# Performance work log

Hardware: AMD Instinct MI355X
Metric: run time of the kernel (lower is better)

The kernel has to match this reference:

```python
import jax, jax.numpy as jnp
from jax import lax
import numpy as np

N, T, D, H, HG, OG = 2048, 256, 16, 256, 256, 128

def setup_inputs() -> dict:
    key = jax.random.key(0)
    ks = jax.random.split(key, 16)
    s = 0.05
    return {
        'x':    jax.random.normal(ks[0], (N, T, D), jnp.float32),
        'Wih0': jax.random.normal(ks[1], (4 * H, D), jnp.float32) * s,
        'Whh0': jax.random.normal(ks[2], (4 * H, H), jnp.float32) * s,
        'bih0': jax.random.normal(ks[3], (4 * H,), jnp.float32) * s,
        'bhh0': jax.random.normal(ks[4], (4 * H,), jnp.float32) * s,
        'Wih1': jax.random.normal(ks[5], (4 * H, H), jnp.float32) * s,
        'Whh1': jax.random.normal(ks[6], (4 * H, H), jnp.float32) * s,
        'bih1': jax.random.normal(ks[7], (4 * H,), jnp.float32) * s,
        'bhh1': jax.random.normal(ks[8], (4 * H,), jnp.float32) * s,
        'Wg1':  jax.random.normal(ks[9], (H, HG), jnp.float32) * s,
        'Wg2':  jax.random.normal(ks[10], (HG, OG), jnp.float32) * s,
        'Wfc':  jax.random.normal(ks[11], (OG, 1), jnp.float32) * s,
        'bfc':  jax.random.normal(ks[12], (1,), jnp.float32) * s,
    }

def lstm_layer(x, Wih, Whh, bih, bhh):
    # x: [N, T, Din]; torch gate order i, f, g, o stacked along 4H
    n = x.shape[0]
    h4 = Whh.shape[0]
    hid = h4 // 4
    xg = jnp.einsum('ntd,gd->ntg', x, Wih) + bih + bhh  # precompute input part
    def step(carry, g_t):
        h, c = carry
        g = g_t + h @ Whh.T
        i, f, gg, o = jnp.split(g, 4, axis=-1)
        c = jax.nn.sigmoid(f) * c + jax.nn.sigmoid(i) * jnp.tanh(gg)
        h = jax.nn.sigmoid(o) * jnp.tanh(c)
        return (h, c), h
    h0 = jnp.zeros((n, hid), x.dtype)
    (_, _), hs = lax.scan(step, (h0, h0), jnp.swapaxes(xg, 0, 1))
    return jnp.swapaxes(hs, 0, 1)  # [N, T, H]

def adjacency(nf):
    # detached correlation graph + symmetric degree normalization
    f = lax.stop_gradient(nf)
    xc = f - f.mean(axis=1, keepdims=True)
    cov = xc @ xc.T
    d = jnp.sqrt(jnp.diag(cov))
    corr = jnp.nan_to_num(jnp.clip(cov / (d[:, None] * d[None, :]), -1.0, 1.0))
    A = corr + jnp.eye(f.shape[0], dtype=f.dtype)
    dinv = jnp.power(A.sum(axis=1), -0.5)
    dinv = jnp.where(jnp.isinf(dinv), 0.0, dinv)
    return dinv[:, None] * A * dinv[None, :]

def reference(x, Wih0, Whh0, bih0, bhh0, Wih1, Whh1, bih1, bhh1, Wg1, Wg2, Wfc, bfc):
    h = lstm_layer(x, Wih0, Whh0, bih0, bhh0)
    h = lstm_layer(h, Wih1, Whh1, bih1, bhh1)
    nf = h[:, -1, :]                      # [N, H]
    adj = adjacency(nf)                   # [N, N]
    g1 = jax.nn.relu(adj @ (nf @ Wg1))    # GCN layer 1 (dropout=0, eval)
    g2 = adj @ (g1 @ Wg2)                 # GCN layer 2
    pred = g2 @ Wfc + bfc                 # [N, 1]
    return pred[:, 0]
```

## Files before the change

kernel.cpp:

```cpp
#include <hip/hip_runtime.h>
#include <hip/hip_bf16.h>
#include <cmath>

#define NN 2048
#define TT 256
#define DD 16
#define HH 256
#define NBLK 512

typedef __attribute__((ext_vector_type(8))) short short8;
typedef __attribute__((ext_vector_type(4))) float f32x4;

__device__ __forceinline__ float sigmoidf_(float x){ return 1.0f/(1.0f+expf(-x)); }

__device__ __forceinline__ void glds16(const __hip_bfloat16* g, __hip_bfloat16* l){
  __builtin_amdgcn_global_load_lds(
      (const __attribute__((address_space(1))) void*)g,
      (__attribute__((address_space(3))) void*)l, 16, 0, 0);
}
__device__ __forceinline__ void glds16_dev(const __hip_bfloat16* g, __hip_bfloat16* l){
  __builtin_amdgcn_global_load_lds(
      (const __attribute__((address_space(1))) void*)g,
      (__attribute__((address_space(3))) void*)l, 16, 0, 17);
}

__global__ __launch_bounds__(256) void pack_w2(const float* __restrict__ W,
                                               __hip_bfloat16* __restrict__ P){
  int tid = blockIdx.x*256 + threadIdx.x;
  int r = tid >> 8, k = tid & 255;
  float w = W[tid];
  __hip_bfloat16 h = __float2bfloat16(w);
  __hip_bfloat16 l = __float2bfloat16(w - __bfloat162float(h));
  size_t base = (size_t)r*512;
  P[base + k] = h; P[base + 256 + k] = l;
}
__global__ __launch_bounds__(256) void pack_w0(const float* __restrict__ W,
                                               __hip_bfloat16* __restrict__ P){
  int tid = blockIdx.x*256 + threadIdx.x;
  int r = tid >> 4, k = tid & 15;
  float w = W[tid];
  __hip_bfloat16 h = __float2bfloat16(w);
  __hip_bfloat16 l = __float2bfloat16(w - __bfloat162float(h));
  size_t base = (size_t)r*64;
  P[base + k] = h; P[base + 16 + k] = h; P[base + 32 + k] = l;
  P[base + 48 + k] = __float2bfloat16(0.0f);
}
__global__ __launch_bounds__(256) void pack_x(const float* __restrict__ x,
                                              __hip_bfloat16* __restrict__ Xp){
  int tid = blockIdx.x*256 + threadIdx.x;
  const float* xr = x + (size_t)tid*16;
  __hip_bfloat16* o = Xp + (size_t)tid*64;
  for (int k=0;k<16;k++){
    float v = xr[k];
    __hip_bfloat16 h = __float2bfloat16(v);
    __hip_bfloat16 l = __float2bfloat16(v - __bfloat162float(h));
    o[k] = h; o[16+k] = l; o[32+k] = h; o[48+k] = __float2bfloat16(0.0f);
  }
}
__global__ __launch_bounds__(256) void recon_nf(const __hip_bfloat16* __restrict__ hi,
    const __hip_bfloat16* __restrict__ lo, float* __restrict__ nf){
  int tid = blockIdx.x*256 + threadIdx.x;
  nf[tid] = __bfloat162float(hi[tid]) + __bfloat162float(lo[tid]);
}

__global__ __launch_bounds__(256) void bar_init(unsigned* __restrict__ bar){
  for (int i = threadIdx.x; i < 2048; i += 256) bar[i] = 0u;
}

__device__ __forceinline__ void lean_sync(unsigned* bar, int t, int bid){
  __syncthreads();
  if (threadIdx.x == 0){
    const int x = bid & 7;
    unsigned a = __hip_atomic_fetch_add(bar + x*16, 1u, __ATOMIC_RELAXED,
                                        __HIP_MEMORY_SCOPE_AGENT);
    if (a == (unsigned)(64u*(t+1) - 1u)){
      unsigned g = __hip_atomic_fetch_add(bar + 128, 1u, __ATOMIC_RELAXED,
                                          __HIP_MEMORY_SCOPE_AGENT);
      if (g == (unsigned)(8u*(t+1) - 1u)){
        #pragma unroll
        for (int i=0;i<8;i++)
          __hip_atomic_store(bar + 1536 + i*64, (unsigned)(t+1),
                             __ATOMIC_RELAXED, __HIP_MEMORY_SCOPE_AGENT);
      } else {
        while (__hip_atomic_load(bar + 1536 + x*64, __ATOMIC_RELAXED,
                                 __HIP_MEMORY_SCOPE_AGENT) < (unsigned)(t+1))
          __builtin_amdgcn_s_sleep(4);
      }
    } else {
      while (__hip_atomic_load(bar + 1536 + x*64, __ATOMIC_RELAXED,
                               __HIP_MEMORY_SCOPE_AGENT) < (unsigned)(t+1))
        __builtin_amdgcn_s_sleep(4);
    }
  }
  __syncthreads();
}

__device__ __forceinline__ void mm_merged(
    const __hip_bfloat16* __restrict__ Ahi, const __hip_bfloat16* __restrict__ Alo,
    size_t lda,
    const __hip_bfloat16* __restrict__ Bhi, const __hip_bfloat16* __restrict__ Blo,
    size_t ldb, int Klen,
    int m0, int j0, int wv, int lane, int rr, int sw8, int frow,
    f32x4 (&acc)[2][4],
    __hip_bfloat16* AsH, __hip_bfloat16* AsL,
    __hip_bfloat16* BsH, __hip_bfloat16* BsL)
{
  const size_t arow = (size_t)(m0 + wv*32 + rr)*lda + sw8;
  const size_t brow = (size_t)(wv*256 + j0 + rr)*ldb + sw8;
  for (int kb=0; kb<Klen; kb+=64){
    {
      const __hip_bfloat16* AbH = Ahi + arow + kb;
      __hip_bfloat16* AdH = AsH + (wv*32)*64;
      #pragma unroll
      for (int c2=0;c2<4;c2++) glds16_dev(AbH + (size_t)(c2*8)*lda, AdH + c2*8*64);
      const __hip_bfloat16* AbL = Alo + arow + kb;
      __hip_bfloat16* AdL = AsL + (wv*32)*64;
      #pragma unroll
      for (int c2=0;c2<4;c2++) glds16_dev(AbL + (size_t)(c2*8)*lda, AdL + c2*8*64);
      const __hip_bfloat16* Bb1 = Bhi + brow + kb;
      __hip_bfloat16* Bd1 = BsH + (wv<<4)*64;
      glds16(Bb1, Bd1); glds16(Bb1 + (size_t)8*ldb, Bd1 + 8*64);
      const __hip_bfloat16* Bb2 = Blo + brow + kb;
      __hip_bfloat16* Bd2 = BsL + (wv<<4)*64;
      glds16(Bb2, Bd2); glds16(Bb2 + (size_t)8*ldb, Bd2 + 8*64);
    }
    __syncthreads();
    #pragma unroll
    for (int w2=0; w2<2; ++w2){
      const int sl8 = ((((w2<<2) + (lane>>4)) ^ (lane&7)) << 3);
      short8 ah0 = *(const short8*)&AsH[(wv*32 +      frow)*64 + sl8];
      short8 ah1 = *(const short8*)&AsH[(wv*32 + 16 + frow)*64 + sl8];
      short8 al0 = *(const short8*)&AsL[(wv*32 +      frow)*64 + sl8];
      short8 al1 = *(const short8*)&AsL[(wv*32 + 16 + frow)*64 + sl8];
      #pragma unroll
      for (int g=0; g<4; ++g){
        short8 bh = *(const short8*)&BsH[((g<<4) + frow)*64 + sl8];
        acc[0][g] = __builtin_amdgcn_mfma_f32_16x16x32_bf16(ah0, bh, acc[0][g], 0,0,0);
        acc[1][g] = __builtin_amdgcn_mfma_f32_16x16x32_bf16(ah1, bh, acc[1][g], 0,0,0);
        acc[0][g] = __builtin_amdgcn_mfma_f32_16x16x32_bf16(al0, bh, acc[0][g], 0,0,0);
        acc[1][g] = __builtin_amdgcn_mfma_f32_16x16x32_bf16(al1, bh, acc[1][g], 0,0,0);
        short8 bl = *(const short8*)&BsL[((g<<4) + frow)*64 + sl8];
        acc[0][g] = __builtin_amdgcn_mfma_f32_16x16x32_bf16(ah0, bl, acc[0][g], 0,0,0);
        acc[1][g] = __builtin_amdgcn_mfma_f32_16x16x32_bf16(ah1, bl, acc[1][g], 0,0,0);
      }
    }
    __syncthreads();
  }
}

__device__ __forceinline__ void mm_single64(
    const __hip_bfloat16* __restrict__ A, size_t lda,
    const __hip_bfloat16* __restrict__ B, size_t ldb,
    int m0, int j0, int wv, int lane, int rr, int sw8, int frow,
    f32x4 (&acc)[2][4],
    __hip_bfloat16* As0, __hip_bfloat16* Bh0)
{
  {
    const __hip_bfloat16* Ab = A + (size_t)(m0 + wv*32 + rr)*lda + sw8;
    __hip_bfloat16* Ad = As0 + (wv*32)*64;
    #pragma unroll
    for (int c2=0;c2<4;c2++) glds16(Ab + (size_t)(c2*8)*lda, Ad + c2*8*64);
    const __hip_bfloat16* Bb1 = B + (size_t)(wv*256 + j0 + rr)*ldb + sw8;
    __hip_bfloat16* Bd1 = Bh0 + (wv<<4)*64;
    glds16(Bb1, Bd1); glds16(Bb1 + (size_t)8*ldb, Bd1 + 8*64);
  }
  __syncthreads();
  #pragma unroll
  for (int w2=0; w2<2; ++w2){
    const int sl8 = ((((w2<<2) + (lane>>4)) ^ (lane&7)) << 3);
    short8 a0 = *(const short8*)&As0[(wv*32 +      frow)*64 + sl8];
    short8 a1 = *(const short8*)&As0[(wv*32 + 16 + frow)*64 + sl8];
    #pragma unroll
    for (int g=0; g<4; ++g){
      short8 b1 = *(const short8*)&Bh0[((g<<4) + frow)*64 + sl8];
      acc[0][g] = __builtin_amdgcn_mfma_f32_16x16x32_bf16(a0, b1, acc[0][g], 0,0,0);
      acc[1][g] = __builtin_amdgcn_mfma_f32_16x16x32_bf16(a1, b1, acc[1][g], 0,0,0);
    }
  }
  __syncthreads();
}

__global__ __launch_bounds__(256, 2) void lstm2_all(
    const __hip_bfloat16* __restrict__ Xp,
    const __hip_bfloat16* __restrict__ P0ih,
    const __hip_bfloat16* __restrict__ P0hh,
    const __hip_bfloat16* __restrict__ P1ih,
    const __hip_bfloat16* __restrict__ P1hh,
    const float* __restrict__ bih0, const float* __restrict__ bhh0,
    const float* __restrict__ bih1, const float* __restrict__ bhh1,
    __hip_bfloat16* __restrict__ H0hi0, __hip_bfloat16* __restrict__ H0lo0,
    __hip_bfloat16* __restrict__ H0hi1, __hip_bfloat16* __restrict__ H0lo1,
    __hip_bfloat16* __restrict__ H1hi0, __hip_bfloat16* __restrict__ H1lo0,
    __hip_bfloat16* __restrict__ H1hi1, __hip_bfloat16* __restrict__ H1lo1,
    unsigned* __restrict__ bar)
{
  __shared__ __align__(16) __hip_bfloat16 AsH[128*64];
  __shared__ __align__(16) __hip_bfloat16 AsL[128*64];
  __shared__ __align__(16) __hip_bfloat16 BsH[64*64];
  __shared__ __align__(16) __hip_bfloat16 BsL[64*64];

  const int bid = blockIdx.x;
  const int xcd = bid & 7;
  const int slot = bid >> 3;
  const bool isL0 = xcd < 4;
  const int lg = isL0 ? xcd : (xcd - 4);
  const int jg = ((lg & 1) << 3) + (slot & 7);
  const int mg = ((lg >> 1) << 3) + (slot >> 3);
  const int m0 = mg << 7;
  const int j0 = jg << 4;
  const int lane = threadIdx.x & 63, wv = threadIdx.x >> 6;
  const int rr = lane >> 3;
  const int sw8 = (((lane & 7) ^ rr) << 3);
  const int frow = lane & 15;
  const int odd = frow & 1;

  const int j = j0 + frow;
  const float* bih = isL0 ? bih0 : bih1;
  const float* bhh = isL0 ? bhh0 : bhh1;
  const float b0 = bih[j]        + bhh[j];
  const float b1 = bih[HH + j]   + bhh[HH + j];
  const float b2 = bih[2*HH + j] + bhh[2*HH + j];
  const float b3 = bih[3*HH + j] + bhh[3*HH + j];

  float creg[2][4] = {{0.f,0.f,0.f,0.f},{0.f,0.f,0.f,0.f}};

  for (int t = 0; t <= TT; ++t){
    const int p = t & 1;
    const bool active = isL0 ? (t < TT) : (t >= 1);
    if (active){
      f32x4 acc[2][4] = {};
      const __hip_bfloat16* h0p_hi = p ? H0hi0 : H0hi1;
      const __hip_bfloat16* h0p_lo = p ? H0lo0 : H0lo1;
      if (isL0){
        if (t != 0){
          mm_merged(h0p_hi, h0p_lo, 256, P0hh, P0hh+256, 512, 256,
                    m0, j0, wv, lane, rr, sw8, frow, acc, AsH, AsL, BsH, BsL);
        }
        mm_single64(Xp + (size_t)t*64, (size_t)TT*64, P0ih, 64,
                    m0, j0, wv, lane, rr, sw8, frow, acc, AsH, BsH);
      } else {
        mm_merged(h0p_hi, h0p_lo, 256, P1ih, P1ih+256, 512, 256,
                  m0, j0, wv, lane, rr, sw8, frow, acc, AsH, AsL, BsH, BsL);
        if (t != 1){
          const __hip_bfloat16* h1p_hi = p ? H1hi1 : H1hi0;
          const __hip_bfloat16* h1p_lo = p ? H1lo1 : H1lo0;
          mm_merged(h1p_hi, h1p_lo, 256, P1hh, P1hh+256, 512, 256,
                    m0, j0, wv, lane, rr, sw8, frow, acc, AsH, AsL, BsH, BsL);
        }
      }
      __hip_bfloat16* ohi = isL0 ? (p ? H0hi1 : H0hi0)
                                 : (p ? H1hi0 : H1hi1);
      __hip_bfloat16* olo = isL0 ? (p ? H0lo1 : H0lo0)
                                 : (p ? H1lo0 : H1lo1);
      #pragma unroll
      for (int mt=0; mt<2; ++mt){
        const int mrb = m0 + wv*32 + mt*16 + ((lane>>4)<<2);
        #pragma unroll
        for (int r=0; r<4; ++r){
          float gi = acc[mt][0][r] + b0;
          float gf = acc[mt][1][r] + b1;
          float gg = acc[mt][2][r] + b2;
          float go = acc[mt][3][r] + b3;
          float cn = sigmoidf_(gf)*creg[mt][r] + sigmoidf_(gi)*tanhf(gg);
          creg[mt][r] = cn;
          float hv = sigmoidf_(go)*tanhf(cn);
          __hip_bfloat16 hb = __float2bfloat16(hv);
          __hip_bfloat16 lb = __float2bfloat16(hv - __bfloat162float(hb));
          unsigned hs = (unsigned)*reinterpret_cast<unsigned short*>(&hb);
          unsigned ls = (unsigned)*reinterpret_cast<unsigned short*>(&lb);
          unsigned hp = (unsigned)__shfl_xor((int)hs, 1);
          unsigned lp = (unsigned)__shfl_xor((int)ls, 1);
          const size_t base = (size_t)(mrb + r)*HH + (size_t)(j & ~1);
          if (!odd){
            unsigned v = hs | (hp << 16);
            __hip_atomic_store((unsigned*)(ohi + base), v,
                               __ATOMIC_RELAXED, __HIP_MEMORY_SCOPE_AGENT);
          } else {
            unsigned v = lp | (ls << 16);
            __hip_atomic_store((unsigned*)(olo + base), v,
                               __ATOMIC_RELAXED, __HIP_MEMORY_SCOPE_AGENT);
          }
        }
      }
    }
    if (t < TT) lean_sync(bar, t, bid);
  }
}

__global__ __launch_bounds__(256) void gemm_nn(
    float* __restrict__ C, const float* __restrict__ A, const float* __restrict__ B,
    int K, int lda, int ldb, int ldc, int relu)
{
  __shared__ float As_[16][68];
  __shared__ float Bs_[16][64];
  float acc[4][4] = {};
  const int tx = threadIdx.x;
  const int m0 = blockIdx.y<<6, n0 = blockIdx.x<<6;
  const int am = tx>>2, ak = (tx&3)<<2;
  const int bk = tx>>4, bn = (tx&15)<<2;
  const int mm = (tx>>4)<<2, nc = (tx&15)<<2;
  for (int kb=0; kb<K; kb+=16){
    float4 av = *reinterpret_cast<const float4*>(A + (size_t)(m0+am)*lda + kb + ak);
    As_[ak][am]=av.x; As_[ak+1][am]=av.y; As_[ak+2][am]=av.z; As_[ak+3][am]=av.w;
    *reinterpret_cast<float4*>(&Bs_[bk][bn]) =
      *reinterpret_cast<const float4*>(B + (size_t)(kb+bk)*ldb + n0 + bn);
    __syncthreads();
    #pragma unroll
    for (int k=0;k<16;k++){
      float4 a4 = *reinterpret_cast<const float4*>(&As_[k][mm]);
      float4 b4 = *reinterpret_cast<const float4*>(&Bs_[k][nc]);
      acc[0][0]=fmaf(a4.x,b4.x,acc[0][0]); acc[0][1]=fmaf(a4.x,b4.y,acc[0][1]);
      acc[0][2]=fmaf(a4.x,b4.z,acc[0][2]); acc[0][3]=fmaf(a4.x,b4.w,acc[0][3]);
      acc[1][0]=fmaf(a4.y,b4.x,acc[1][0]); acc[1][1]=fmaf(a4.y,b4.y,acc[1][1]);
      acc[1][2]=fmaf(a4.y,b4.z,acc[1][2]); acc[1][3]=fmaf(a4.y,b4.w,acc[1][3]);
      acc[2][0]=fmaf(a4.z,b4.x,acc[2][0]); acc[2][1]=fmaf(a4.z,b4.y,acc[2][1]);
      acc[2][2]=fmaf(a4.z,b4.z,acc[2][2]); acc[2][3]=fmaf(a4.z,b4.w,acc[2][3]);
      acc[3][0]=fmaf(a4.w,b4.x,acc[3][0]); acc[3][1]=fmaf(a4.w,b4.y,acc[3][1]);
      acc[3][2]=fmaf(a4.w,b4.z,acc[3][2]); acc[3][3]=fmaf(a4.w,b4.w,acc[3][3]);
    }
    __syncthreads();
  }
  #pragma unroll
  for (int r=0;r<4;r++){
    float4 v = make_float4(acc[r][0],acc[r][1],acc[r][2],acc[r][3]);
    if (relu){ v.x=fmaxf(v.x,0.f); v.y=fmaxf(v.y,0.f); v.z=fmaxf(v.z,0.f); v.w=fmaxf(v.w,0.f); }
    *reinterpret_cast<float4*>(C + (size_t)(m0+mm+r)*ldc + n0 + nc) = v;
  }
}

__global__ __launch_bounds__(256) void gemm_nt(
    float* __restrict__ C, const float* __restrict__ A, const float* __restrict__ B,
    int K, int lda, int ldb, int ldc)
{
  __shared__ float As_[16][68];
  __shared__ float Bs_[16][68];
  float acc[4][4] = {};
  const int tx = threadIdx.x;
  const int m0 = blockIdx.y<<6, n0 = blockIdx.x<<6;
  const int am = tx>>2, ak = (tx&3)<<2;
  const int mm = (tx>>4)<<2, nc = (tx&15)<<2;
  for (int kb=0; kb<K; kb+=16){
    float4 av = *reinterpret_cast<const float4*>(A + (size_t)(m0+am)*lda + kb + ak);
    As_[ak][am]=av.x; As_[ak+1][am]=av.y; As_[ak+2][am]=av.z; As_[ak+3][am]=av.w;
    float4 bv = *reinterpret_cast<const float4*>(B + (size_t)(n0+am)*ldb + kb + ak);
    Bs_[ak][am]=bv.x; Bs_[ak+1][am]=bv.y; Bs_[ak+2][am]=bv.z; Bs_[ak+3][am]=bv.w;
    __syncthreads();
    #pragma unroll
    for (int k=0;k<16;k++){
      float4 a4 = *reinterpret_cast<const float4*>(&As_[k][mm]);
      float4 b4 = *reinterpret_cast<const float4*>(&Bs_[k][nc]);
      acc[0][0]=fmaf(a4.x,b4.x,acc[0][0]); acc[0][1]=fmaf(a4.x,b4.y,acc[0][1]);
      acc[0][2]=fmaf(a4.x,b4.z,acc[0][2]); acc[0][3]=fmaf(a4.x,b4.w,acc[0][3]);
      acc[1][0]=fmaf(a4.y,b4.x,acc[1][0]); acc[1][1]=fmaf(a4.y,b4.y,acc[1][1]);
      acc[1][2]=fmaf(a4.y,b4.z,acc[1][2]); acc[1][3]=fmaf(a4.y,b4.w,acc[1][3]);
      acc[2][0]=fmaf(a4.z,b4.x,acc[2][0]); acc[2][1]=fmaf(a4.z,b4.y,acc[2][1]);
      acc[2][2]=fmaf(a4.z,b4.z,acc[2][2]); acc[2][3]=fmaf(a4.z,b4.w,acc[2][3]);
      acc[3][0]=fmaf(a4.w,b4.x,acc[3][0]); acc[3][1]=fmaf(a4.w,b4.y,acc[3][1]);
      acc[3][2]=fmaf(a4.w,b4.z,acc[3][2]); acc[3][3]=fmaf(a4.w,b4.w,acc[3][3]);
    }
    __syncthreads();
  }
  #pragma unroll
  for (int r=0;r<4;r++){
    float4 v = make_float4(acc[r][0],acc[r][1],acc[r][2],acc[r][3]);
    *reinterpret_cast<float4*>(C + (size_t)(m0+mm+r)*ldc + n0 + nc) = v;
  }
}

__global__ __launch_bounds__(256) void rowstat(const float* __restrict__ nf,
    float* __restrict__ xc, float* __restrict__ dvec)
{
  __shared__ float red[256];
  int n = blockIdx.x, tx = threadIdx.x;
  float v = nf[(size_t)n*HH + tx];
  red[tx] = v; __syncthreads();
  for (int s=128; s>0; s>>=1){ if (tx<s) red[tx]+=red[tx+s]; __syncthreads(); }
  float mean = red[0] * (1.0f/HH);
  __syncthreads();
  float d = v - mean;
  xc[(size_t)n*HH + tx] = d;
  red[tx] = d*d; __syncthreads();
  for (int s=128; s>0; s>>=1){ if (tx<s) red[tx]+=red[tx+s]; __syncthreads(); }
  if (tx==0) dvec[n] = sqrtf(red[0]);
}

__global__ __launch_bounds__(256) void rowsum(const float* __restrict__ cov,
    const float* __restrict__ dvec, float* __restrict__ dinv)
{
  __shared__ float red[256];
  int i = blockIdx.x, tx = threadIdx.x;
  float di = dvec[i];
  float s = 0.f;
  for (int jj=tx; jj<NN; jj+=256){
    float r = cov[(size_t)i*NN + jj] / (di * dvec[jj]);
    if (r != r) r = 0.f; else r = fminf(1.f, fmaxf(-1.f, r));
    s += r;
  }
  red[tx]=s; __syncthreads();
  for (int st=128; st>0; st>>=1){ if (tx<st) red[tx]+=red[tx+st]; __syncthreads(); }
  if (tx==0){
    float tot = red[0] + 1.0f;
    float p = powf(tot, -0.5f);
    if (isinf(p)) p = 0.f;
    dinv[i] = p;
  }
}

__global__ __launch_bounds__(256) void adjnorm(float* __restrict__ cov,
    const float* __restrict__ dvec, const float* __restrict__ dinv)
{
  size_t idx = (size_t)blockIdx.x*256 + threadIdx.x;
  int i = (int)(idx >> 11), jj = (int)(idx & (NN-1));
  float r = cov[idx] / (dvec[i]*dvec[jj]);
  if (r != r) r = 0.f; else r = fminf(1.f, fmaxf(-1.f, r));
  if (i==jj) r += 1.f;
  cov[idx] = dinv[i]*r*dinv[jj];
}

__global__ __launch_bounds__(128) void predk(const float* __restrict__ G2,
    const float* __restrict__ Wfc, const float* __restrict__ bfc, float* __restrict__ out)
{
  int n = blockIdx.x, tx = threadIdx.x;
  float v = G2[(size_t)n*128 + tx] * Wfc[tx];
  for (int off=32; off>0; off>>=1) v += __shfl_down(v, off);
  __shared__ float p[2];
  if ((tx&63)==0) p[tx>>6] = v;
  __syncthreads();
  if (tx==0) out[n] = p[0] + p[1] + bfc[0];
}

extern "C" void kernel_launch(void* const* d_in, const int* in_sizes, int n_in,
                              void* d_out, int out_size, void* d_ws, size_t ws_size,
                              hipStream_t stream)
{
  const float* x    = (const float*)d_in[0];
  const float* Wih0 = (const float*)d_in[1];
  const float* Whh0 = (const float*)d_in[2];
  const float* bih0 = (const float*)d_in[3];
  const float* bhh0 = (const float*)d_in[4];
  const float* Wih1 = (const float*)d_in[5];
  const float* Whh1 = (const float*)d_in[6];
  const float* bih1 = (const float*)d_in[7];
  const float* bhh1 = (const float*)d_in[8];
  const float* Wg1  = (const float*)d_in[9];
  const float* Wg2  = (const float*)d_in[10];
  const float* Wfc  = (const float*)d_in[11];
  const float* bfc  = (const float*)d_in[12];
  float* out = (float*)d_out;

  char* w = (char*)d_ws;
  auto alloc = [&](size_t bytes){ char* p = w; w += (bytes + 255) & ~(size_t)255; return p; };
  __hip_bfloat16* Xp   = (__hip_bfloat16*)alloc((size_t)NN*TT*64*2);
  __hip_bfloat16* P0hh = (__hip_bfloat16*)alloc((size_t)1024*512*2);
  __hip_bfloat16* P1ih = (__hip_bfloat16*)alloc((size_t)1024*512*2);
  __hip_bfloat16* P1hh = (__hip_bfloat16*)alloc((size_t)1024*512*2);
  __hip_bfloat16* P0ih = (__hip_bfloat16*)alloc((size_t)1024*64*2);
  __hip_bfloat16 *H0hi[2], *H0lo[2], *H1hi[2], *H1lo[2];
  for (int i=0;i<2;i++){ H0hi[i]=(__hip_bfloat16*)alloc((size_t)NN*HH*2);
                         H0lo[i]=(__hip_bfloat16*)alloc((size_t)NN*HH*2); }
  for (int i=0;i<2;i++){ H1hi[i]=(__hip_bfloat16*)alloc((size_t)NN*HH*2);
                         H1lo[i]=(__hip_bfloat16*)alloc((size_t)NN*HH*2); }
  float* nf   = (float*)alloc((size_t)NN*HH*4);
  float* xc   = (float*)alloc((size_t)NN*HH*4);
  float* cov  = (float*)alloc((size_t)NN*NN*4);
  float* t1   = (float*)alloc((size_t)NN*HH*4);
  float* G1   = (float*)alloc((size_t)NN*HH*4);
  float* t2   = (float*)alloc((size_t)NN*128*4);
  float* G2   = (float*)alloc((size_t)NN*128*4);
  float* dvec = (float*)alloc((size_t)NN*4);
  float* dinv = (float*)alloc((size_t)NN*4);
  unsigned* bar = (unsigned*)alloc(8192);

  hipLaunchKernelGGL(bar_init, dim3(1), dim3(256), 0, stream, bar);
  hipLaunchKernelGGL(pack_w2, dim3(1024), dim3(256), 0, stream, Whh0, P0hh);
  hipLaunchKernelGGL(pack_w2, dim3(1024), dim3(256), 0, stream, Wih1, P1ih);
  hipLaunchKernelGGL(pack_w2, dim3(1024), dim3(256), 0, stream, Whh1, P1hh);
  hipLaunchKernelGGL(pack_w0, dim3(64),   dim3(256), 0, stream, Wih0, P0ih);
  hipLaunchKernelGGL(pack_x,  dim3(2048), dim3(256), 0, stream, x, Xp);

  hipLaunchKernelGGL(lstm2_all, dim3(NBLK), dim3(256), 0, stream,
      Xp, P0ih, P0hh, P1ih, P1hh, bih0, bhh0, bih1, bhh1,
      H0hi[0], H0lo[0], H0hi[1], H0lo[1],
      H1hi[0], H1lo[0], H1hi[1], H1lo[1], bar);

  hipLaunchKernelGGL(recon_nf, dim3(2048), dim3(256), 0, stream, H1hi[1], H1lo[1], nf);

  hipLaunchKernelGGL(rowstat, dim3(NN), dim3(256), 0, stream, nf, xc, dvec);
  hipLaunchKernelGGL(gemm_nt, dim3(NN/64, NN/64), dim3(256), 0, stream,
      cov, xc, xc, HH, HH, HH, NN);
  hipLaunchKernelGGL(rowsum, dim3(NN), dim3(256), 0, stream, cov, dvec, dinv);
  hipLaunchKernelGGL(adjnorm, dim3(NN*NN/256), dim3(256), 0, stream, cov, dvec, dinv);

  hipLaunchKernelGGL(gemm_nn, dim3(HH/64, NN/64), dim3(256), 0, stream,
      t1, nf, Wg1, HH, HH, HH, HH, 0);
  hipLaunchKernelGGL(gemm_nn, dim3(HH/64, NN/64), dim3(256), 0, stream,
      G1, cov, t1, NN, NN, HH, HH, 1);
  hipLaunchKernelGGL(gemm_nn, dim3(128/64, NN/64), dim3(256), 0, stream,
      t2, G1, Wg2, HH, HH, 128, 128, 0);
  hipLaunchKernelGGL(gemm_nn, dim3(128/64, NN/64), dim3(256), 0, stream,
      G2, cov, t2, NN, NN, 128, 128, 0);
  hipLaunchKernelGGL(predk, dim3(NN), dim3(128), 0, stream, G2, Wfc, bfc, out);
}
```

Before: 4.648 ms.

## Merge both LSTM layers into every block, sharing the h0 tile across layers

Blocks are no longer split into a layer-0 half and a layer-1 half. Each block now computes both layers for a 64-row by 16-column tile. The h0(t-1) tile loaded into LDS is reused for both the layer-0 recurrent GEMM and the layer-1 input GEMM, which removes a duplicate load of the h0 activations. This halves the rows per block and adds a third B buffer in LDS. Per-block work now covers both layers, which may change load balance and how fast the barrier is reached.

New measurement: 6.843 ms. 1.47x slower.

```diff
diff --git a/kernel.cpp b/kernel.cpp
--- a/kernel.cpp
+++ b/kernel.cpp
@@ -95,91 +95,6 @@
   __syncthreads();
 }
 
-__device__ __forceinline__ void mm_merged(
-    const __hip_bfloat16* __restrict__ Ahi, const __hip_bfloat16* __restrict__ Alo,
-    size_t lda,
-    const __hip_bfloat16* __restrict__ Bhi, const __hip_bfloat16* __restrict__ Blo,
-    size_t ldb, int Klen,
-    int m0, int j0, int wv, int lane, int rr, int sw8, int frow,
-    f32x4 (&acc)[2][4],
-    __hip_bfloat16* AsH, __hip_bfloat16* AsL,
-    __hip_bfloat16* BsH, __hip_bfloat16* BsL)
-{
-  const size_t arow = (size_t)(m0 + wv*32 + rr)*lda + sw8;
-  const size_t brow = (size_t)(wv*256 + j0 + rr)*ldb + sw8;
-  for (int kb=0; kb<Klen; kb+=64){
-    {
-      const __hip_bfloat16* AbH = Ahi + arow + kb;
-      __hip_bfloat16* AdH = AsH + (wv*32)*64;
-      #pragma unroll
-      for (int c2=0;c2<4;c2++) glds16_dev(AbH + (size_t)(c2*8)*lda, AdH + c2*8*64);
-      const __hip_bfloat16* AbL = Alo + arow + kb;
-      __hip_bfloat16* AdL = AsL + (wv*32)*64;
-      #pragma unroll
-      for (int c2=0;c2<4;c2++) glds16_dev(AbL + (size_t)(c2*8)*lda, AdL + c2*8*64);
-      const __hip_bfloat16* Bb1 = Bhi + brow + kb;
-      __hip_bfloat16* Bd1 = BsH + (wv<<4)*64;
-      glds16(Bb1, Bd1); glds16(Bb1 + (size_t)8*ldb, Bd1 + 8*64);
-      const __hip_bfloat16* Bb2 = Blo + brow + kb;
-      __hip_bfloat16* Bd2 = BsL + (wv<<4)*64;
-      glds16(Bb2, Bd2); glds16(Bb2 + (size_t)8*ldb, Bd2 + 8*64);
-    }
-    __syncthreads();
-    #pragma unroll
-    for (int w2=0; w2<2; ++w2){
-      const int sl8 = ((((w2<<2) + (lane>>4)) ^ (lane&7)) << 3);
-      short8 ah0 = *(const short8*)&AsH[(wv*32 +      frow)*64 + sl8];
-      short8 ah1 = *(const short8*)&AsH[(wv*32 + 16 + frow)*64 + sl8];
-      short8 al0 = *(const short8*)&AsL[(wv*32 +      frow)*64 + sl8];
-      short8 al1 = *(const short8*)&AsL[(wv*32 + 16 + frow)*64 + sl8];
-      #pragma unroll
-      for (int g=0; g<4; ++g){
-        short8 bh = *(const short8*)&BsH[((g<<4) + frow)*64 + sl8];
-        acc[0][g] = __builtin_amdgcn_mfma_f32_16x16x32_bf16(ah0, bh, acc[0][g], 0,0,0);
-        acc[1][g] = __builtin_amdgcn_mfma_f32_16x16x32_bf16(ah1, bh, acc[1][g], 0,0,0);
-        acc[0][g] = __builtin_amdgcn_mfma_f32_16x16x32_bf16(al0, bh, acc[0][g], 0,0,0);
-        acc[1][g] = __builtin_amdgcn_mfma_f32_16x16x32_bf16(al1, bh, acc[1][g], 0,0,0);
-        short8 bl = *(const short8*)&BsL[((g<<4) + frow)*64 + sl8];
-        acc[0][g] = __builtin_amdgcn_mfma_f32_16x16x32_bf16(ah0, bl, acc[0][g], 0,0,0);
-        acc[1][g] = __builtin_amdgcn_mfma_f32_16x16x32_bf16(ah1, bl, acc[1][g], 0,0,0);
-      }
-    }
-    __syncthreads();
-  }
-}
-
-__device__ __forceinline__ void mm_single64(
-    const __hip_bfloat16* __restrict__ A, size_t lda,
-    const __hip_bfloat16* __restrict__ B, size_t ldb,
-    int m0, int j0, int wv, int lane, int rr, int sw8, int frow,
-    f32x4 (&acc)[2][4],
-    __hip_bfloat16* As0, __hip_bfloat16* Bh0)
-{
-  {
-    const __hip_bfloat16* Ab = A + (size_t)(m0 + wv*32 + rr)*lda + sw8;
-    __hip_bfloat16* Ad = As0 + (wv*32)*64;
-    #pragma unroll
-    for (int c2=0;c2<4;c2++) glds16(Ab + (size_t)(c2*8)*lda, Ad + c2*8*64);
-    const __hip_bfloat16* Bb1 = B + (size_t)(wv*256 + j0 + rr)*ldb + sw8;
-    __hip_bfloat16* Bd1 = Bh0 + (wv<<4)*64;
-    glds16(Bb1, Bd1); glds16(Bb1 + (size_t)8*ldb, Bd1 + 8*64);
-  }
-  __syncthreads();
-  #pragma unroll
-  for (int w2=0; w2<2; ++w2){
-    const int sl8 = ((((w2<<2) + (lane>>4)) ^ (lane&7)) << 3);
-    short8 a0 = *(const short8*)&As0[(wv*32 +      frow)*64 + sl8];
-    short8 a1 = *(const short8*)&As0[(wv*32 + 16 + frow)*64 + sl8];
-    #pragma unroll
-    for (int g=0; g<4; ++g){
-      short8 b1 = *(const short8*)&Bh0[((g<<4) + frow)*64 + sl8];
-      acc[0][g] = __builtin_amdgcn_mfma_f32_16x16x32_bf16(a0, b1, acc[0][g], 0,0,0);
-      acc[1][g] = __builtin_amdgcn_mfma_f32_16x16x32_bf16(a1, b1, acc[1][g], 0,0,0);
-    }
-  }
-  __syncthreads();
-}
-
 __global__ __launch_bounds__(256, 2) void lstm2_all(
     const __hip_bfloat16* __restrict__ Xp,
     const __hip_bfloat16* __restrict__ P0ih,
@@ -194,19 +109,19 @@
     __hip_bfloat16* __restrict__ H1hi1, __hip_bfloat16* __restrict__ H1lo1,
     unsigned* __restrict__ bar)
 {
-  __shared__ __align__(16) __hip_bfloat16 AsH[128*64];
-  __shared__ __align__(16) __hip_bfloat16 AsL[128*64];
-  __shared__ __align__(16) __hip_bfloat16 BsH[64*64];
-  __shared__ __align__(16) __hip_bfloat16 BsL[64*64];
+  __shared__ __align__(16) __hip_bfloat16 AsH[64*64];
+  __shared__ __align__(16) __hip_bfloat16 AsL[64*64];
+  __shared__ __align__(16) __hip_bfloat16 B0H[64*64];
+  __shared__ __align__(16) __hip_bfloat16 B0L[64*64];
+  __shared__ __align__(16) __hip_bfloat16 B1H[64*64];
+  __shared__ __align__(16) __hip_bfloat16 B1L[64*64];
 
   const int bid = blockIdx.x;
   const int xcd = bid & 7;
   const int slot = bid >> 3;
-  const bool isL0 = xcd < 4;
-  const int lg = isL0 ? xcd : (xcd - 4);
-  const int jg = ((lg & 1) << 3) + (slot & 7);
-  const int mg = ((lg >> 1) << 3) + (slot >> 3);
-  const int m0 = mg << 7;
+  const int jg = (xcd << 1) | (slot & 1);
+  const int mg = slot >> 1;
+  const int m0 = mg << 6;
   const int j0 = jg << 4;
   const int lane = threadIdx.x & 63, wv = threadIdx.x >> 6;
   const int rr = lane >> 3;
@@ -215,71 +130,185 @@
   const int odd = frow & 1;
 
   const int j = j0 + frow;
-  const float* bih = isL0 ? bih0 : bih1;
-  const float* bhh = isL0 ? bhh0 : bhh1;
-  const float b0 = bih[j]        + bhh[j];
-  const float b1 = bih[HH + j]   + bhh[HH + j];
-  const float b2 = bih[2*HH + j] + bhh[2*HH + j];
-  const float b3 = bih[3*HH + j] + bhh[3*HH + j];
-
-  float creg[2][4] = {{0.f,0.f,0.f,0.f},{0.f,0.f,0.f,0.f}};
+  const float b00 = bih0[j]        + bhh0[j];
+  const float b01 = bih0[HH + j]   + bhh0[HH + j];
+  const float b02 = bih0[2*HH + j] + bhh0[2*HH + j];
+  const float b03 = bih0[3*HH + j] + bhh0[3*HH + j];
+  const float b10 = bih1[j]        + bhh1[j];
+  const float b11 = bih1[HH + j]   + bhh1[HH + j];
+  const float b12 = bih1[2*HH + j] + bhh1[2*HH + j];
+  const float b13 = bih1[3*HH + j] + bhh1[3*HH + j];
+
+  float creg0[4] = {0.f,0.f,0.f,0.f};
+  float creg1[4] = {0.f,0.f,0.f,0.f};
+
+  const size_t arow = (size_t)(m0 + wv*16 + rr);
+  const size_t brow = (size_t)(wv*256 + j0 + rr);
+  const int ldsA = (wv*16)*64;
+  const int ldsB = (wv<<4)*64;
 
   for (int t = 0; t <= TT; ++t){
     const int p = t & 1;
-    const bool active = isL0 ? (t < TT) : (t >= 1);
-    if (active){
-      f32x4 acc[2][4] = {};
+    const bool doL0 = (t < TT);
+    f32x4 acc0[4] = {};
+    f32x4 acc1[4] = {};
+
+    if (t >= 1){
       const __hip_bfloat16* h0p_hi = p ? H0hi0 : H0hi1;
       const __hip_bfloat16* h0p_lo = p ? H0lo0 : H0lo1;
-      if (isL0){
-        if (t != 0){
-          mm_merged(h0p_hi, h0p_lo, 256, P0hh, P0hh+256, 512, 256,
-                    m0, j0, wv, lane, rr, sw8, frow, acc, AsH, AsL, BsH, BsL);
+      const size_t ar = arow*256 + sw8;
+      const size_t br = brow*512 + sw8;
+      for (int kb=0; kb<256; kb+=64){
+        glds16_dev(h0p_hi + ar + kb,                 AsH + ldsA);
+        glds16_dev(h0p_hi + ar + (size_t)8*256 + kb, AsH + ldsA + 8*64);
+        glds16_dev(h0p_lo + ar + kb,                 AsL + ldsA);
+        glds16_dev(h0p_lo + ar + (size_t)8*256 + kb, AsL + ldsA + 8*64);
+        if (doL0){
+          glds16(P0hh + br + kb,                     B0H + ldsB);
+          glds16(P0hh + br + (size_t)8*512 + kb,     B0H + ldsB + 8*64);
+          glds16(P0hh + 256 + br + kb,               B0L + ldsB);
+          glds16(P0hh + 256 + br + (size_t)8*512 + kb, B0L + ldsB + 8*64);
         }
-        mm_single64(Xp + (size_t)t*64, (size_t)TT*64, P0ih, 64,
-                    m0, j0, wv, lane, rr, sw8, frow, acc, AsH, BsH);
-      } else {
-        mm_merged(h0p_hi, h0p_lo, 256, P1ih, P1ih+256, 512, 256,
-                  m0, j0, wv, lane, rr, sw8, frow, acc, AsH, AsL, BsH, BsL);
-        if (t != 1){
-          const __hip_bfloat16* h1p_hi = p ? H1hi1 : H1hi0;
-          const __hip_bfloat16* h1p_lo = p ? H1lo1 : H1lo0;
-          mm_merged(h1p_hi, h1p_lo, 256, P1hh, P1hh+256, 512, 256,
-                    m0, j0, wv, lane, rr, sw8, frow, acc, AsH, AsL, BsH, BsL);
+        glds16(P1ih + br + kb,                       B1H + ldsB);
+        glds16(P1ih + br + (size_t)8*512 + kb,       B1H + ldsB + 8*64);
+        glds16(P1ih + 256 + br + kb,                 B1L + ldsB);
+        glds16(P1ih + 256 + br + (size_t)8*512 + kb, B1L + ldsB + 8*64);
+        __syncthreads();
+        #pragma unroll
+        for (int w2=0; w2<2; ++w2){
+          const int sl8 = ((((w2<<2) + (lane>>4)) ^ (lane&7)) << 3);
+          short8 ah = *(const short8*)&AsH[(wv*16 + frow)*64 + sl8];
+          short8 al = *(const short8*)&AsL[(wv*16 + frow)*64 + sl8];
+          #pragma unroll
+          for (int g=0; g<4; ++g){
+            if (doL0){
+              short8 bh = *(const short8*)&B0H[((g<<4) + frow)*64 + sl8];
+              acc0[g] = __builtin_amdgcn_mfma_f32_16x16x32_bf16(ah, bh, acc0[g], 0,0,0);
+              acc0[g] = __builtin_amdgcn_mfma_f32_16x16x32_bf16(al, bh, acc0[g], 0,0,0);
+              short8 bl = *(const short8*)&B0L[((g<<4) + frow)*64 + sl8];
+              acc0[g] = __builtin_amdgcn_mfma_f32_16x16x32_bf16(ah, bl, acc0[g], 0,0,0);
+            }
+            short8 bh1 = *(const short8*)&B1H[((g<<4) + frow)*64 + sl8];
+            acc1[g] = __builtin_amdgcn_mfma_f32_16x16x32_bf16(ah, bh1, acc1[g], 0,0,0);
+            acc1[g] = __builtin_amdgcn_mfma_f32_16x16x32_bf16(al, bh1, acc1[g], 0,0,0);
+            short8 bl1 = *(const short8*)&B1L[((g<<4) + frow)*64 + sl8];
+            acc1[g] = __builtin_amdgcn_mfma_f32_16x16x32_bf16(ah, bl1, acc1[g], 0,0,0);
+          }
+        }
+        __syncthreads();
+      }
+      if (t >= 2){
+        const __hip_bfloat16* h1p_hi = p ? H1hi1 : H1hi0;
+        const __hip_bfloat16* h1p_lo = p ? H1lo1 : H1lo0;
+        const size_t ar1 = arow*256 + sw8;
+        for (int kb=0; kb<256; kb+=64){
+          glds16_dev(h1p_hi + ar1 + kb,                 AsH + ldsA);
+          glds16_dev(h1p_hi + ar1 + (size_t)8*256 + kb, AsH + ldsA + 8*64);
+          glds16_dev(h1p_lo + ar1 + kb,                 AsL + ldsA);
+          glds16_dev(h1p_lo + ar1 + (size_t)8*256 + kb, AsL + ldsA + 8*64);
+          glds16(P1hh + br + kb,                        B0H + ldsB);
+          glds16(P1hh + br + (size_t)8*512 + kb,        B0H + ldsB + 8*64);
+          glds16(P1hh + 256 + br + kb,                  B0L + ldsB);
+          glds16(P1hh + 256 + br + (size_t)8*512 + kb,  B0L + ldsB + 8*64);
+          __syncthreads();
+          #pragma unroll
+          for (int w2=0; w2<2; ++w2){
+            const int sl8 = ((((w2<<2) + (lane>>4)) ^ (lane&7)) << 3);
+            short8 ah = *(const short8*)&AsH[(wv*16 + frow)*64 + sl8];
+            short8 al = *(const short8*)&AsL[(wv*16 + frow)*64 + sl8];
+            #pragma unroll
+            for (int g=0; g<4; ++g){
+              short8 bh = *(const short8*)&B0H[((g<<4) + frow)*64 + sl8];
+              acc1[g] = __builtin_amdgcn_mfma_f32_16x16x32_bf16(ah, bh, acc1[g], 0,0,0);
+              acc1[g] = __builtin_amdgcn_mfma_f32_16x16x32_bf16(al, bh, acc1[g], 0,0,0);
+              short8 bl = *(const short8*)&B0L[((g<<4) + frow)*64 + sl8];
+              acc1[g] = __builtin_amdgcn_mfma_f32_16x16x32_bf16(ah, bl, acc1[g], 0,0,0);
+            }
+          }
+          __syncthreads();
         }
       }
-      __hip_bfloat16* ohi = isL0 ? (p ? H0hi1 : H0hi0)
-                                 : (p ? H1hi0 : H1hi1);
-      __hip_bfloat16* olo = isL0 ? (p ? H0lo1 : H0lo0)
-                                 : (p ? H1lo0 : H1lo1);
+    }
+    if (doL0){
+      const size_t arx = arow*((size_t)TT*64) + sw8;
+      const size_t brx = brow*64 + sw8;
+      const __hip_bfloat16* Xb = Xp + (size_t)t*64;
+      glds16(Xb + arx,                          AsH + ldsA);
+      glds16(Xb + arx + (size_t)8*TT*64,        AsH + ldsA + 8*64);
+      glds16(P0ih + brx,                        B0H + ldsB);
+      glds16(P0ih + brx + (size_t)8*64,         B0H + ldsB + 8*64);
+      __syncthreads();
       #pragma unroll
-      for (int mt=0; mt<2; ++mt){
-        const int mrb = m0 + wv*32 + mt*16 + ((lane>>4)<<2);
+      for (int w2=0; w2<2; ++w2){
+        const int sl8 = ((((w2<<2) + (lane>>4)) ^ (lane&7)) << 3);
+        short8 a0 = *(const short8*)&AsH[(wv*16 + frow)*64 + sl8];
         #pragma unroll
-        for (int r=0; r<4; ++r){
-          float gi = acc[mt][0][r] + b0;
-          float gf = acc[mt][1][r] + b1;
-          float gg = acc[mt][2][r] + b2;
-          float go = acc[mt][3][r] + b3;
-          float cn = sigmoidf_(gf)*creg[mt][r] + sigmoidf_(gi)*tanhf(gg);
-          creg[mt][r] = cn;
-          float hv = sigmoidf_(go)*tanhf(cn);
-          __hip_bfloat16 hb = __float2bfloat16(hv);
-          __hip_bfloat16 lb = __float2bfloat16(hv - __bfloat162float(hb));
-          unsigned hs = (unsigned)*reinterpret_cast<unsigned short*>(&hb);
-          unsigned ls = (unsigned)*reinterpret_cast<unsigned short*>(&lb);
-          unsigned hp = (unsigned)__shfl_xor((int)hs, 1);
-          unsigned lp = (unsigned)__shfl_xor((int)ls, 1);
-          const size_t base = (size_t)(mrb + r)*HH + (size_t)(j & ~1);
-          if (!odd){
-            unsigned v = hs | (hp << 16);
-            __hip_atomic_store((unsigned*)(ohi + base), v,
-                               __ATOMIC_RELAXED, __HIP_MEMORY_SCOPE_AGENT);
-          } else {
-            unsigned v = lp | (ls << 16);
-            __hip_atomic_store((unsigned*)(olo + base), v,
-                               __ATOMIC_RELAXED, __HIP_MEMORY_SCOPE_AGENT);
-          }
+        for (int g=0; g<4; ++g){
+          short8 b1 = *(const short8*)&B0H[((g<<4) + frow)*64 + sl8];
+          acc0[g] = __builtin_amdgcn_mfma_f32_16x16x32_bf16(a0, b1, acc0[g], 0,0,0);
+        }
+      }
+      __syncthreads();
+    }
+
+    const int mrb = m0 + wv*16 + ((lane>>4)<<2);
+    if (doL0){
+      __hip_bfloat16* ohi = p ? H0hi1 : H0hi0;
+      __hip_bfloat16* olo = p ? H0lo1 : H0lo0;
+      #pragma unroll
+      for (int r=0; r<4; ++r){
+        float gi = acc0[0][r] + b00;
+        float gf = acc0[1][r] + b01;
+        float gg = acc0[2][r] + b02;
+        float go = acc0[3][r] + b03;
+        float cn = sigmoidf_(gf)*creg0[r] + sigmoidf_(gi)*tanhf(gg);
+        creg0[r] = cn;
+        float hv = sigmoidf_(go)*tanhf(cn);
+        __hip_bfloat16 hb = __float2bfloat16(hv);
+        __hip_bfloat16 lb = __float2bfloat16(hv - __bfloat162float(hb));
+        unsigned hs = (unsigned)*reinterpret_cast<unsigned short*>(&hb);
+        unsigned ls = (unsigned)*reinterpret_cast<unsigned short*>(&lb);
+        unsigned hp = (unsigned)__shfl_xor((int)hs, 1);
+        unsigned lp = (unsigned)__shfl_xor((int)ls, 1);
+        const size_t base = (size_t)(mrb + r)*HH + (size_t)(j & ~1);
+        if (!odd){
+          unsigned v = hs | (hp << 16);
+          __hip_atomic_store((unsigned*)(ohi + base), v,
+                             __ATOMIC_RELAXED, __HIP_MEMORY_SCOPE_AGENT);
+        } else {
+          unsigned v = lp | (ls << 16);
+          __hip_atomic_store((unsigned*)(olo + base), v,
+                             __ATOMIC_RELAXED, __HIP_MEMORY_SCOPE_AGENT);
+        }
+      }
+    }
+    if (t >= 1){
+      __hip_bfloat16* ohi = p ? H1hi0 : H1hi1;
+      __hip_bfloat16* olo = p ? H1lo0 : H1lo1;
+      #pragma unroll
+      for (int r=0; r<4; ++r){
+        float gi = acc1[0][r] + b10;
+        float gf = acc1[1][r] + b11;
+        float gg = acc1[2][r] + b12;
+        float go = acc1[3][r] + b13;
+        float cn = sigmoidf_(gf)*creg1[r] + sigmoidf_(gi)*tanhf(gg);
+        creg1[r] = cn;
+        float hv = sigmoidf_(go)*tanhf(cn);
+        __hip_bfloat16 hb = __float2bfloat16(hv);
+        __hip_bfloat16 lb = __float2bfloat16(hv - __bfloat162float(hb));
+        unsigned hs = (unsigned)*reinterpret_cast<unsigned short*>(&hb);
+        unsigned ls = (unsigned)*reinterpret_cast<unsigned short*>(&lb);
+        unsigned hp = (unsigned)__shfl_xor((int)hs, 1);
+        unsigned lp = (unsigned)__shfl_xor((int)ls, 1);
+        const size_t base = (size_t)(mrb + r)*HH + (size_t)(j & ~1);
+        if (!odd){
+          unsigned v = hs | (hp << 16);
+          __hip_atomic_store((unsigned*)(ohi + base), v,
+                             __ATOMIC_RELAXED, __HIP_MEMORY_SCOPE_AGENT);
+        } else {
+          unsigned v = lp | (ls << 16);
+          __hip_atomic_store((unsigned*)(olo + base), v,
+                             __ATOMIC_RELAXED, __HIP_MEMORY_SCOPE_AGENT);
         }
       }
     }
```

## Double-buffer A tiles in recurrent LSTM matmul to overlap loads with MFMA

Applied to the files above, without the earlier changes.

Replaces the load-sync-compute-sync K loop in the merged hi/lo matmul with a software pipeline. A tiles are double-buffered in LDS, the next chunk's loads are issued while the current one computes, and partial vmcnt waits plus raw s_barrier replace full __syncthreads. This aims to hide global-to-LDS latency in the latency-bound per-timestep recurrence. It doubles A-tile LDS use (now about 80KB per block), which may conflict with the two-blocks-per-CU launch bound, and it relies on hand-counted vmcnt values being correct.

Result: no change. 4.726 ms (+1.7%).

```diff
diff --git a/kernel.cpp b/kernel.cpp
--- a/kernel.cpp
+++ b/kernel.cpp
@@ -95,56 +95,93 @@
   __syncthreads();
 }
 
-__device__ __forceinline__ void mm_merged(
+__device__ __forceinline__ void stageA_pl(
+    const __hip_bfloat16* Ahi, const __hip_bfloat16* Alo, size_t arow, size_t lda,
+    int kb, __hip_bfloat16* dH, __hip_bfloat16* dL, int wv)
+{
+  const __hip_bfloat16* AbH = Ahi + arow + kb;
+  __hip_bfloat16* AdH = dH + (wv*32)*64;
+  #pragma unroll
+  for (int c2=0;c2<4;c2++) glds16_dev(AbH + (size_t)(c2*8)*lda, AdH + c2*8*64);
+  const __hip_bfloat16* AbL = Alo + arow + kb;
+  __hip_bfloat16* AdL = dL + (wv*32)*64;
+  #pragma unroll
+  for (int c2=0;c2<4;c2++) glds16_dev(AbL + (size_t)(c2*8)*lda, AdL + c2*8*64);
+}
+__device__ __forceinline__ void stageB_pl(
+    const __hip_bfloat16* Bhi, const __hip_bfloat16* Blo, size_t brow, size_t ldb,
+    int kb, __hip_bfloat16* BsH, __hip_bfloat16* BsL, int wv)
+{
+  const __hip_bfloat16* Bb1 = Bhi + brow + kb;
+  __hip_bfloat16* Bd1 = BsH + (wv<<4)*64;
+  glds16(Bb1, Bd1); glds16(Bb1 + (size_t)8*ldb, Bd1 + 8*64);
+  const __hip_bfloat16* Bb2 = Blo + brow + kb;
+  __hip_bfloat16* Bd2 = BsL + (wv<<4)*64;
+  glds16(Bb2, Bd2); glds16(Bb2 + (size_t)8*ldb, Bd2 + 8*64);
+}
+__device__ __forceinline__ void mfma_chunk(
+    const __hip_bfloat16* AH, const __hip_bfloat16* AL,
+    const __hip_bfloat16* BsH, const __hip_bfloat16* BsL,
+    f32x4 (&acc)[2][4], int lane, int wv, int frow)
+{
+  #pragma unroll
+  for (int w2=0; w2<2; ++w2){
+    const int sl8 = ((((w2<<2) + (lane>>4)) ^ (lane&7)) << 3);
+    short8 ah0 = *(const short8*)&AH[(wv*32 +      frow)*64 + sl8];
+    short8 ah1 = *(const short8*)&AH[(wv*32 + 16 + frow)*64 + sl8];
+    short8 al0 = *(const short8*)&AL[(wv*32 +      frow)*64 + sl8];
+    short8 al1 = *(const short8*)&AL[(wv*32 + 16 + frow)*64 + sl8];
+    #pragma unroll
+    for (int g=0; g<4; ++g){
+      short8 bh = *(const short8*)&BsH[((g<<4) + frow)*64 + sl8];
+      acc[0][g] = __builtin_amdgcn_mfma_f32_16x16x32_bf16(ah0, bh, acc[0][g], 0,0,0);
+      acc[1][g] = __builtin_amdgcn_mfma_f32_16x16x32_bf16(ah1, bh, acc[1][g], 0,0,0);
+      acc[0][g] = __builtin_amdgcn_mfma_f32_16x16x32_bf16(al0, bh, acc[0][g], 0,0,0);
+      acc[1][g] = __builtin_amdgcn_mfma_f32_16x16x32_bf16(al1, bh, acc[1][g], 0,0,0);
+      short8 bl = *(const short8*)&BsL[((g<<4) + frow)*64 + sl8];
+      acc[0][g] = __builtin_amdgcn_mfma_f32_16x16x32_bf16(ah0, bl, acc[0][g], 0,0,0);
+      acc[1][g] = __builtin_amdgcn_mfma_f32_16x16x32_bf16(ah1, bl, acc[1][g], 0,0,0);
+    }
+  }
+}
+
+__device__ __forceinline__ void mm_merged_pl(
     const __hip_bfloat16* __restrict__ Ahi, const __hip_bfloat16* __restrict__ Alo,
     size_t lda,
     const __hip_bfloat16* __restrict__ Bhi, const __hip_bfloat16* __restrict__ Blo,
-    size_t ldb, int Klen,
+    size_t ldb,
     int m0, int j0, int wv, int lane, int rr, int sw8, int frow,
     f32x4 (&acc)[2][4],
-    __hip_bfloat16* AsH, __hip_bfloat16* AsL,
+    __hip_bfloat16* AsH0, __hip_bfloat16* AsL0,
+    __hip_bfloat16* AsH1, __hip_bfloat16* AsL1,
     __hip_bfloat16* BsH, __hip_bfloat16* BsL)
 {
   const size_t arow = (size_t)(m0 + wv*32 + rr)*lda + sw8;
   const size_t brow = (size_t)(wv*256 + j0 + rr)*ldb + sw8;
-  for (int kb=0; kb<Klen; kb+=64){
-    {
-      const __hip_bfloat16* AbH = Ahi + arow + kb;
-      __hip_bfloat16* AdH = AsH + (wv*32)*64;
-      #pragma unroll
-      for (int c2=0;c2<4;c2++) glds16_dev(AbH + (size_t)(c2*8)*lda, AdH + c2*8*64);
-      const __hip_bfloat16* AbL = Alo + arow + kb;
-      __hip_bfloat16* AdL = AsL + (wv*32)*64;
-      #pragma unroll
-      for (int c2=0;c2<4;c2++) glds16_dev(AbL + (size_t)(c2*8)*lda, AdL + c2*8*64);
-      const __hip_bfloat16* Bb1 = Bhi + brow + kb;
-      __hip_bfloat16* Bd1 = BsH + (wv<<4)*64;
-      glds16(Bb1, Bd1); glds16(Bb1 + (size_t)8*ldb, Bd1 + 8*64);
-      const __hip_bfloat16* Bb2 = Blo + brow + kb;
-      __hip_bfloat16* Bd2 = BsL + (wv<<4)*64;
-      glds16(Bb2, Bd2); glds16(Bb2 + (size_t)8*ldb, Bd2 + 8*64);
-    }
-    __syncthreads();
-    #pragma unroll
-    for (int w2=0; w2<2; ++w2){
-      const int sl8 = ((((w2<<2) + (lane>>4)) ^ (lane&7)) << 3);
-      short8 ah0 = *(const short8*)&AsH[(wv*32 +      frow)*64 + sl8];
-      short8 ah1 = *(const short8*)&AsH[(wv*32 + 16 + frow)*64 + sl8];
-      short8 al0 = *(const short8*)&AsL[(wv*32 +      frow)*64 + sl8];
-      short8 al1 = *(const short8*)&AsL[(wv*32 + 16 + frow)*64 + sl8];
-      #pragma unroll
-      for (int g=0; g<4; ++g){
-        short8 bh = *(const short8*)&BsH[((g<<4) + frow)*64 + sl8];
-        acc[0][g] = __builtin_amdgcn_mfma_f32_16x16x32_bf16(ah0, bh, acc[0][g], 0,0,0);
-        acc[1][g] = __builtin_amdgcn_mfma_f32_16x16x32_bf16(ah1, bh, acc[1][g], 0,0,0);
-        acc[0][g] = __builtin_amdgcn_mfma_f32_16x16x32_bf16(al0, bh, acc[0][g], 0,0,0);
-        acc[1][g] = __builtin_amdgcn_mfma_f32_16x16x32_bf16(al1, bh, acc[1][g], 0,0,0);
-        short8 bl = *(const short8*)&BsL[((g<<4) + frow)*64 + sl8];
-        acc[0][g] = __builtin_amdgcn_mfma_f32_16x16x32_bf16(ah0, bl, acc[0][g], 0,0,0);
-        acc[1][g] = __builtin_amdgcn_mfma_f32_16x16x32_bf16(ah1, bl, acc[1][g], 0,0,0);
+  stageA_pl(Ahi, Alo, arow, lda, 0,  AsH0, AsL0, wv);
+  stageB_pl(Bhi, Blo, brow, ldb, 0,  BsH, BsL, wv);
+  stageA_pl(Ahi, Alo, arow, lda, 64, AsH1, AsL1, wv);
+  asm volatile("s_waitcnt vmcnt(8)" ::: "memory");
+  __builtin_amdgcn_sched_barrier(0);
+  __builtin_amdgcn_s_barrier();
+  #pragma unroll
+  for (int c=0; c<4; ++c){
+    const __hip_bfloat16* AH = (c&1) ? AsH1 : AsH0;
+    const __hip_bfloat16* AL = (c&1) ? AsL1 : AsL0;
+    mfma_chunk(AH, AL, BsH, BsL, acc, lane, wv, frow);
+    __builtin_amdgcn_s_barrier();
+    if (c < 3){
+      stageB_pl(Bhi, Blo, brow, ldb, (c+1)*64, BsH, BsL, wv);
+      if (c < 2){
+        stageA_pl(Ahi, Alo, arow, lda, (c+2)*64,
+                  (c&1) ? AsH1 : AsH0, (c&1) ? AsL1 : AsL0, wv);
+        asm volatile("s_waitcnt vmcnt(8)" ::: "memory");
+      } else {
+        asm volatile("s_waitcnt vmcnt(0)" ::: "memory");
       }
-    }
-    __syncthreads();
+      __builtin_amdgcn_sched_barrier(0);
+      __builtin_amdgcn_s_barrier();
+    }
   }
 }
 
@@ -194,8 +231,10 @@
     __hip_bfloat16* __restrict__ H1hi1, __hip_bfloat16* __restrict__ H1lo1,
     unsigned* __restrict__ bar)
 {
-  __shared__ __align__(16) __hip_bfloat16 AsH[128*64];
-  __shared__ __align__(16) __hip_bfloat16 AsL[128*64];
+  __shared__ __align__(16) __hip_bfloat16 AsH0[128*64];
+  __shared__ __align__(16) __hip_bfloat16 AsL0[128*64];
+  __shared__ __align__(16) __hip_bfloat16 AsH1[128*64];
+  __shared__ __align__(16) __hip_bfloat16 AsL1[128*64];
   __shared__ __align__(16) __hip_bfloat16 BsH[64*64];
   __shared__ __align__(16) __hip_bfloat16 BsL[64*64];
 
@@ -233,19 +272,22 @@
       const __hip_bfloat16* h0p_lo = p ? H0lo0 : H0lo1;
       if (isL0){
         if (t != 0){
-          mm_merged(h0p_hi, h0p_lo, 256, P0hh, P0hh+256, 512, 256,
-                    m0, j0, wv, lane, rr, sw8, frow, acc, AsH, AsL, BsH, BsL);
+          mm_merged_pl(h0p_hi, h0p_lo, 256, P0hh, P0hh+256, 512,
+                       m0, j0, wv, lane, rr, sw8, frow, acc,
+                       AsH0, AsL0, AsH1, AsL1, BsH, BsL);
         }
         mm_single64(Xp + (size_t)t*64, (size_t)TT*64, P0ih, 64,
-                    m0, j0, wv, lane, rr, sw8, frow, acc, AsH, BsH);
+                    m0, j0, wv, lane, rr, sw8, frow, acc, AsH0, BsH);
       } else {
-        mm_merged(h0p_hi, h0p_lo, 256, P1ih, P1ih+256, 512, 256,
-                  m0, j0, wv, lane, rr, sw8, frow, acc, AsH, AsL, BsH, BsL);
+        mm_merged_pl(h0p_hi, h0p_lo, 256, P1ih, P1ih+256, 512,
+                     m0, j0, wv, lane, rr, sw8, frow, acc,
+                     AsH0, AsL0, AsH1, AsL1, BsH, BsL);
         if (t != 1){
           const __hip_bfloat16* h1p_hi = p ? H1hi1 : H1hi0;
           const __hip_bfloat16* h1p_lo = p ? H1lo1 : H1lo0;
-          mm_merged(h1p_hi, h1p_lo, 256, P1hh, P1hh+256, 512, 256,
-                    m0, j0, wv, lane, rr, sw8, frow, acc, AsH, AsL, BsH, BsL);
+          mm_merged_pl(h1p_hi, h1p_lo, 256, P1hh, P1hh+256, 512,
+                       m0, j0, wv, lane, rr, sw8, frow, acc,
+                       AsH0, AsL0, AsH1, AsL1, BsH, BsL);
         }
       }
       __hip_bfloat16* ohi = isL0 ? (p ? H0hi1 : H0hi0)
```
